# Kernel optimization log

Hardware: AMD Instinct MI355X
Metric: run time of the kernel (lower is better)

## Reference

```python
import jax, jax.numpy as jnp
import numpy as np

N_NODES = 50000
N_EDGES = 800000
NEG_SLOPE = 0.2


def _gat_layer(x, src, dst, W, a_src, a_dst, bias, heads, out_ch):
    """PyG-style GATConv with self-loops already appended to src/dst."""
    N = x.shape[0]
    h = (x @ W.T).reshape(N, heads, out_ch)            # [N,H,C]
    alpha_src = jnp.einsum('nhc,hc->nh', h, a_src)      # [N,H]
    alpha_dst = jnp.einsum('nhc,hc->nh', h, a_dst)      # [N,H]
    e = jax.nn.leaky_relu(alpha_src[src] + alpha_dst[dst], NEG_SLOPE)  # [E,H]
    # segment softmax over incoming edges of each destination node
    m = jax.ops.segment_max(e, dst, num_segments=N)     # [N,H]
    ex = jnp.exp(e - m[dst])
    denom = jax.ops.segment_sum(ex, dst, num_segments=N)  # [N,H] (>0: self-loops)
    alpha = ex / (denom[dst] + 1e-16)                    # [E,H]
    out = jax.ops.segment_sum(h[src] * alpha[:, :, None], dst, num_segments=N)  # [N,H,C]
    return out.reshape(N, heads * out_ch) + bias


def _with_self_loops(edge_index, n):
    loop = jnp.arange(n, dtype=edge_index.dtype)
    src = jnp.concatenate([edge_index[0], loop])
    dst = jnp.concatenate([edge_index[1], loop])
    return src, dst


def setup_inputs() -> dict:
    key = jax.random.key(0)
    ks = jax.random.split(key, 12)
    s = lambda fan: 1.0 / np.sqrt(fan)
    return {
        'x': jax.random.normal(ks[0], (N_NODES, 16), jnp.float32),
        'edge_index': jax.random.randint(ks[1], (2, N_EDGES), 0, N_NODES, jnp.int64),
        'W1': jax.random.normal(ks[2], (256, 16), jnp.float32) * s(16),
        'att_src1': jax.random.normal(ks[3], (4, 64), jnp.float32) * s(64),
        'att_dst1': jax.random.normal(ks[4], (4, 64), jnp.float32) * s(64),
        'b1': jnp.zeros((256,), jnp.float32),
        'W2': jax.random.normal(ks[5], (64, 256), jnp.float32) * s(256),
        'att_src2': jax.random.normal(ks[6], (1, 64), jnp.float32) * s(64),
        'att_dst2': jax.random.normal(ks[7], (1, 64), jnp.float32) * s(64),
        'b2': jnp.zeros((64,), jnp.float32),
        'fc_w': jax.random.normal(ks[8], (1, 64), jnp.float32) * s(64),
        'fc_b': jnp.zeros((1,), jnp.float32),
    }


def reference(x, edge_index, W1, att_src1, att_dst1, b1,
              W2, att_src2, att_dst2, b2, fc_w, fc_b):
    src, dst = _with_self_loops(edge_index, x.shape[0])
    h = jax.nn.elu(_gat_layer(x, src, dst, W1, att_src1, att_dst1, b1, heads=4, out_ch=64))
    h = jax.nn.elu(_gat_layer(h, src, dst, W2, att_src2, att_dst2, b2, heads=1, out_ch=64))
    return h @ fc_w.T + fc_b
```

## Files before the change

kernel.cpp:

```cpp
#include <hip/hip_runtime.h>
#include <hip/hip_bf16.h>
#include <stdint.h>

#define N_NODES 50000
#define N_EDGES 800000
#define MAXDEG  96
#define NSLICE  6250
#define NSB     196

#define OFF_X    0
#define OFF_W1   800000
#define OFF_AS1  804096
#define OFF_AD1  804352
#define OFF_B1   804608
#define OFF_W2   804864
#define OFF_AS2  821248
#define OFF_AD2  821312
#define OFF_B2   821376
#define OFF_FCW  821440
#define OFF_FCB  821504
#define N_CANON  821505
#define N_W2B    16384
#define N_W1B    16384
#define N_CONV   (N_CANON + N_W2B + N_W1B + N_NODES)

#define TSTRIDE 264

typedef __hip_bfloat16 bf16;
typedef __attribute__((ext_vector_type(8))) short short8;
typedef __attribute__((ext_vector_type(4))) float f32x4;

__device__ __forceinline__ float b2f(bf16 v){ return (float)v; }
__device__ __forceinline__ int clampi(int v, int lo, int hi){ return v < lo ? lo : (v > hi ? hi : v); }
__device__ __forceinline__ float clampf(float v){ return fminf(fmaxf(v, -40.f), 40.f); }
__device__ __forceinline__ uint16_t f2bfbits(float f){
  union { float f; uint32_t u; } c; c.f = f;
  uint32_t r = c.u + 0x7fff + ((c.u >> 16) & 1);
  return (uint16_t)(r >> 16);
}
__device__ __forceinline__ float bitsf(uint32_t u){
  union { uint32_t u; float f; } c; c.u = u; return c.f;
}
__device__ __forceinline__ uint32_t fbits(float f){
  union { float f; uint32_t u; } c; c.f = f; return c.u;
}

__device__ __forceinline__ int load_src(const int* ei, int i, int f){
  return f ? ei[2*(size_t)i] : ei[i];
}
__device__ __forceinline__ int load_dst(const int* ei, int i, int f){
  return f ? ei[2*((size_t)N_EDGES + i)] : ei[N_EDGES + i];
}

__global__ void k_detect(const int* __restrict__ ei, const uint16_t* __restrict__ xu,
                         int* __restrict__ flag){
  const int l = threadIdx.x;
  int or_odd = ei[2*l + 1] | ei[2*(400000 + l) + 1];
  int hits = 0;
  for(int k = 0; k < 64; k++){
    int e = (xu[l*64 + k] >> 7) & 0xFF;
    hits += (e >= 200);
  }
  #pragma unroll
  for(int off=32; off; off>>=1){
    or_odd |= __shfl_xor(or_odd, off, 64);
    hits   += __shfl_xor(hits,   off, 64);
  }
  if(l == 0){
    flag[0] = (or_odd == 0) ? 1 : 0;
    flag[1] = (hits > 16) ? 1 : 0;
  }
}

__global__ void k_convert(const void* x, const void* W1, const void* as1w, const void* ad1w,
                          const void* b1, const void* W2, const void* as2w, const void* ad2w,
                          const void* b2, const void* fcw, const void* fcb,
                          float* __restrict__ canon, uint16_t* __restrict__ W2b,
                          uint16_t* __restrict__ W1b, int* __restrict__ cnt,
                          int* __restrict__ csr_pad, const int* __restrict__ flag){
  int i = blockIdx.x*256 + threadIdx.x;
  int fp32 = flag[1];
  if(i >= N_CANON + N_W2B + N_W1B){
    int j = i - (N_CANON + N_W2B + N_W1B);
    if(j < N_NODES){ cnt[j] = 1; csr_pad[(size_t)j*MAXDEG] = j; }
    return;
  }
  if(i >= N_CANON + N_W2B){
    int j2 = i - (N_CANON + N_W2B);
    int j = j2 >> 6, kk = j2 & 63;
    uint16_t v = 0;
    if((kk >> 4) == (j >> 6)){
      int e = j*16 + (kk & 15);
      v = fp32 ? f2bfbits(((const float*)W1)[e]) : ((const uint16_t*)W1)[e];
    }
    W1b[j2] = v;
    return;
  }
  if(i >= N_CANON){
    int j = i - N_CANON;
    W2b[j] = fp32 ? f2bfbits(((const float*)W2)[j]) : ((const uint16_t*)W2)[j];
    return;
  }
  const void* src; int off;
  if     (i < OFF_W1 ){ src = x;    off = i; }
  else if(i < OFF_AS1){ src = W1;   off = i - OFF_W1; }
  else if(i < OFF_AD1){ src = as1w; off = i - OFF_AS1; }
  else if(i < OFF_B1 ){ src = ad1w; off = i - OFF_AD1; }
  else if(i < OFF_W2 ){ src = b1;   off = i - OFF_B1; }
  else if(i < OFF_AS2){ src = W2;   off = i - OFF_W2; }
  else if(i < OFF_AD2){ src = as2w; off = i - OFF_AS2; }
  else if(i < OFF_B2 ){ src = ad2w; off = i - OFF_AD2; }
  else if(i < OFF_FCW){ src = b2;   off = i - OFF_B2; }
  else if(i < OFF_FCB){ src = fcw;  off = i - OFF_FCW; }
  else               { src = fcb;  off = 0; }
  float v = fp32 ? ((const float*)src)[off] : b2f(((const bf16*)src)[off]);
  canon[i] = v;
}


__global__ __launch_bounds__(256) void k_prepscat(const float* __restrict__ canon,
                        uint32_t* __restrict__ pack, float* __restrict__ dpack,
                        const int* __restrict__ ei, int* __restrict__ cnt,
                        int* __restrict__ csr_pad, const int* __restrict__ flag){
  const int tid = threadIdx.x;
  if(blockIdx.x >= 196){
    const int bid = blockIdx.x - 196;
    const int grp = bid & 7, sb = bid >> 3;
    const int f = flag[0];
    const int lo = grp*NSLICE, hi = lo + NSLICE;
    const int base = sb*4096;
    #pragma unroll
    for(int j = 0; j < 8; j++){
      int i = base + j*512 + tid*2;
      if(i >= N_EDGES) break;
      int d0, d1;
      if(f){
        int4 dd = *(const int4*)(ei + 2*((size_t)N_EDGES + i));
        d0 = dd.x; d1 = dd.z;
      }else{
        int2 dd = *(const int2*)(ei + N_EDGES + i);
        d0 = dd.x; d1 = dd.y;
      }
      d0 = clampi(d0, 0, N_NODES-1);
      d1 = clampi(d1, 0, N_NODES-1);
      if(d0 >= lo && d0 < hi){
        int s = clampi(load_src(ei, i, f), 0, N_NODES-1);
        int pos = atomicAdd(&cnt[d0], 1);
        pos = clampi(pos, 0, MAXDEG-1);
        csr_pad[(size_t)d0*MAXDEG + pos] = s;
      }
      if(d1 >= lo && d1 < hi){
        int s = clampi(load_src(ei, i+1, f), 0, N_NODES-1);
        int pos = atomicAdd(&cnt[d1], 1);
        pos = clampi(pos, 0, MAXDEG-1);
        csr_pad[(size_t)d1*MAXDEG + pos] = s;
      }
    }
    return;
  }
  __shared__ float ps[64], pd[64];
  if(tid < 128){
    int e = tid & 63;
    int h = e >> 4, k = e & 15;
    const float* av = canon + (tid < 64 ? OFF_AS1 : OFF_AD1) + h*64;
    const float* Wp = canon + OFF_W1 + (h*64)*16 + k;
    float acc = 0.f;
    #pragma unroll 8
    for(int c = 0; c < 64; c++) acc += av[c] * Wp[c*16];
    (tid < 64 ? ps : pd)[e] = acc;
  }
  __syncthreads();
  int n = blockIdx.x*256 + tid;
  if(n >= N_NODES) return;
  float xr[16];
  const float4* xp = (const float4*)(canon + OFF_X + n*16);
  #pragma unroll
  for(int t=0;t<4;t++){ float4 v = xp[t]; xr[4*t]=v.x; xr[4*t+1]=v.y; xr[4*t+2]=v.z; xr[4*t+3]=v.w; }
  uint32_t w[16];
  #pragma unroll
  for(int t=0;t<8;t++)
    w[t] = (uint32_t)f2bfbits(xr[2*t]) | ((uint32_t)f2bfbits(xr[2*t+1]) << 16);
  float qs[8];
  #pragma unroll
  for(int h=0;h<4;h++){
    float a=0.f, b=0.f;
    #pragma unroll
    for(int k=0;k<16;k++){ a += ps[h*16+k]*xr[k]; b += pd[h*16+k]*xr[k]; }
    a = clampf(a); b = clampf(b);
    w[8+2*h]  = fbits(__expf(a));
    w[9+2*h]  = fbits(__expf(0.2f*a));
    qs[2*h]   = __expf(b);
    qs[2*h+1] = __expf(0.2f*b);
  }
  uint4* dst = (uint4*)(pack + (size_t)n*16);
  dst[0] = make_uint4(w[0],w[1],w[2],w[3]);
  dst[1] = make_uint4(w[4],w[5],w[6],w[7]);
  dst[2] = make_uint4(w[8],w[9],w[10],w[11]);
  dst[3] = make_uint4(w[12],w[13],w[14],w[15]);
  float4* dd = (float4*)(dpack + (size_t)n*8);
  dd[0] = make_float4(qs[0],qs[1],qs[2],qs[3]);
  dd[1] = make_float4(qs[4],qs[5],qs[6],qs[7]);
}


struct Ay { float y0,y1,y2,y3,d0,d1,d2,d3; };

__device__ __forceinline__ void edge_acc(const char* __restrict__ r, int k,
                                         float4 qa, float4 qb, bool valid, Ay& a){
  float xv = bitsf((uint32_t)(*(const uint16_t*)(r + k*2)) << 16);
  float4 pa = *(const float4*)(r + 32);
  float4 pb = *(const float4*)(r + 48);
  float w0 = fmaxf(pa.x*qa.x, pa.y*qa.y);
  float w1 = fmaxf(pa.z*qa.z, pa.w*qa.w);
  float w2 = fmaxf(pb.x*qb.x, pb.y*qb.y);
  float w3 = fmaxf(pb.z*qb.z, pb.w*qb.w);
  if(!valid){ w0 = 0.f; w1 = 0.f; w2 = 0.f; w3 = 0.f; }
  a.y0 += w0*xv; a.d0 += w0;
  a.y1 += w1*xv; a.d1 += w1;
  a.y2 += w2*xv; a.d2 += w2;
  a.y3 += w3*xv; a.d3 += w3;
}

__global__ __launch_bounds__(256) void k_aggy(const int* __restrict__ cnt, const int* __restrict__ csr_pad,
                       const uint32_t* __restrict__ pack, const float* __restrict__ dpack,
                       uint16_t* __restrict__ yb){
  const int wv = threadIdx.x >> 6, lane = threadIdx.x & 63;
  const int g = lane >> 4, k = lane & 15;
  const char* pk = (const char*)pack;

  for(int n = blockIdx.x*4 + wv; n < N_NODES; n += gridDim.x*4){
    const int beg = n*MAXDEG;
    const int deg = cnt[n];
    const int end = beg + (deg < MAXDEG ? deg : MAXDEG);
    const float4 qa = *(const float4*)(dpack + (size_t)n*8);
    const float4 qb = *(const float4*)(dpack + (size_t)n*8 + 4);
    Ay a = {0,0,0,0,0,0,0,0};
    int i0 = beg;
    const int nfull = (end - beg) >> 3;
    if(nfull > 0){
      int iA = csr_pad[i0 + g], iB = csr_pad[i0 + 4 + g];
      for(int b = 1; b < nfull; b++){
        int jA = csr_pad[i0 + 8 + g], jB = csr_pad[i0 + 12 + g];
        edge_acc(pk + (size_t)iA*64, k, qa, qb, true, a);
        edge_acc(pk + (size_t)iB*64, k, qa, qb, true, a);
        iA = jA; iB = jB;
        i0 += 8;
      }
      edge_acc(pk + (size_t)iA*64, k, qa, qb, true, a);
      edge_acc(pk + (size_t)iB*64, k, qa, qb, true, a);
      i0 += 8;
    }
    if(i0 < end){
      int iiA = i0 + g, iiB = i0 + 4 + g;
      bool vA = iiA < end, vB = iiB < end;
      int iA = csr_pad[vA ? iiA : end-1];
      int iB = csr_pad[vB ? iiB : end-1];
      edge_acc(pk + (size_t)iA*64, k, qa, qb, vA, a);
      edge_acc(pk + (size_t)iB*64, k, qa, qb, vB, a);
    }
    a.y0 += __shfl_xor(a.y0,16,64); a.y0 += __shfl_xor(a.y0,32,64);
    a.y1 += __shfl_xor(a.y1,16,64); a.y1 += __shfl_xor(a.y1,32,64);
    a.y2 += __shfl_xor(a.y2,16,64); a.y2 += __shfl_xor(a.y2,32,64);
    a.y3 += __shfl_xor(a.y3,16,64); a.y3 += __shfl_xor(a.y3,32,64);
    a.d0 += __shfl_xor(a.d0,16,64); a.d0 += __shfl_xor(a.d0,32,64);
    a.d1 += __shfl_xor(a.d1,16,64); a.d1 += __shfl_xor(a.d1,32,64);
    a.d2 += __shfl_xor(a.d2,16,64); a.d2 += __shfl_xor(a.d2,32,64);
    a.d3 += __shfl_xor(a.d3,16,64); a.d3 += __shfl_xor(a.d3,32,64);
    float yH = (g==0) ? a.y0 : (g==1) ? a.y1 : (g==2) ? a.y2 : a.y3;
    float dH = (g==0) ? a.d0 : (g==1) ? a.d1 : (g==2) ? a.d2 : a.d3;
    yb[(size_t)n*64 + g*16 + k] = f2bfbits(yH / (dH + 1e-16f));
  }
}


__global__ __launch_bounds__(64, 4) void k_mlp(const uint16_t* __restrict__ yb,
                        const uint16_t* __restrict__ W1b, const uint16_t* __restrict__ W2b,
                        const float* __restrict__ canon,
                        bf16* __restrict__ h2, float2* __restrict__ pq2, float2* __restrict__ dq2){
  __shared__ uint16_t tl[16*TSTRIDE];
  const int lane = threadIdx.x & 63;
  const int quad = lane >> 4, c = lane & 15;
  const int n0 = blockIdx.x * 16;

  float b1v[16];
  #pragma unroll
  for(int cb=0; cb<16; cb++) b1v[cb] = canon[OFF_B1 + cb*16 + c];
  float asj[4], adj[4];
  #pragma unroll
  for(int cb=0; cb<4; cb++){
    asj[cb] = canon[OFF_AS2 + cb*16 + c];
    adj[cb] = canon[OFF_AD2 + cb*16 + c];
  }

  short8 af0 = *(const short8*)(yb + (size_t)(n0 + c)*64 + quad*8);
  short8 af1 = *(const short8*)(yb + (size_t)(n0 + c)*64 + 32 + quad*8);
  #pragma unroll
  for(int cb=0; cb<16; cb++){
    short8 wf = *(const short8*)(W1b + (cb*16 + c)*64 + (cb>>3)*32 + quad*8);
    f32x4 acc = (f32x4){0.f,0.f,0.f,0.f};
    acc = __builtin_amdgcn_mfma_f32_16x16x32_bf16((cb>>3) ? af1 : af0, wf, acc, 0,0,0);
    #pragma unroll
    for(int r=0; r<4; r++){
      float o = acc[r] + b1v[cb];
      o = (o > 0.f) ? o : (__expf(o) - 1.f);
      tl[(quad*4 + r)*TSTRIDE + cb*16 + c] = f2bfbits(o);
    }
  }
  f32x4 acc2[4];
  #pragma unroll
  for(int cb=0; cb<4; cb++) acc2[cb] = (f32x4){0.f,0.f,0.f,0.f};
  #pragma unroll
  for(int ks=0; ks<8; ks++){
    short8 af = *(const short8*)(tl + c*TSTRIDE + ks*32 + quad*8);
    #pragma unroll
    for(int cb=0; cb<4; cb++){
      short8 bfrag = *(const short8*)(W2b + (cb*16 + c)*256 + ks*32 + quad*8);
      acc2[cb] = __builtin_amdgcn_mfma_f32_16x16x32_bf16(af, bfrag, acc2[cb], 0,0,0);
    }
  }
  float vs[4] = {0.f,0.f,0.f,0.f}, vd[4] = {0.f,0.f,0.f,0.f};
  #pragma unroll
  for(int cb=0; cb<4; cb++)
    #pragma unroll
    for(int r=0; r<4; r++){
      float v = acc2[cb][r];
      h2[(size_t)(n0 + quad*4 + r)*64 + cb*16 + c] = __float2bfloat16(v);
      vs[r] += v * asj[cb];
      vd[r] += v * adj[cb];
    }
  #pragma unroll
  for(int r=0; r<4; r++){
    #pragma unroll
    for(int off=1; off<16; off<<=1){
      vs[r] += __shfl_xor(vs[r], off, 64);
      vd[r] += __shfl_xor(vd[r], off, 64);
    }
  }
  if(c == 0){
    #pragma unroll
    for(int r=0; r<4; r++){
      float s = clampf(vs[r]), d = clampf(vd[r]);
      pq2[n0 + quad*4 + r] = make_float2(__expf(s), __expf(0.2f*s));
      dq2[n0 + quad*4 + r] = make_float2(__expf(d), __expf(0.2f*d));
    }
  }
}


__global__ __launch_bounds__(256) void k_agg2(const int* __restrict__ cnt, const int* __restrict__ csr_pad,
                       const bf16* __restrict__ h2, const float2* __restrict__ pq2,
                       const float2* __restrict__ dq2, const float* __restrict__ canon,
                       void* __restrict__ outv, const int* __restrict__ flag){
  const int wv = threadIdx.x >> 6, lane = threadIdx.x & 63;
  const int g = lane >> 4, k = lane & 15;
  const char* h2b = (const char*)h2;
  float4 b2v = ((const float4*)(canon + OFF_B2))[k];
  float4 fcv = ((const float4*)(canon + OFF_FCW))[k];
  const float fcb0 = canon[OFF_FCB];
  const int ofp32 = flag[1];
  for(int n = blockIdx.x*4 + wv; n < N_NODES; n += gridDim.x*4){
    const int beg = n*MAXDEG;
    int dg = cnt[n]; dg = dg < MAXDEG ? dg : MAXDEG;
    const int end = beg + dg;
    const float2 qn = dq2[n];
    float a0=0.f,a1=0.f,a2=0.f,a3=0.f, den=0.f;
    int i0 = beg;
    const int nfull = (end - beg) >> 3;
    if(nfull > 0){
      int iA = csr_pad[i0 + g], iB = csr_pad[i0 + 4 + g];
      for(int b = 1; b < nfull; b++){
        int nA = csr_pad[i0 + 8 + g], nB = csr_pad[i0 + 12 + g];
        uint2 hA = *(const uint2*)(h2b + (size_t)iA*128 + k*8);
        float2 pA = pq2[iA];
        uint2 hB = *(const uint2*)(h2b + (size_t)iB*128 + k*8);
        float2 pB = pq2[iB];
        float wA = fmaxf(pA.x*qn.x, pA.y*qn.y);
        float wB = fmaxf(pB.x*qn.x, pB.y*qn.y);
        den += wA + wB;
        a0 += wA*bitsf(hA.x << 16) + wB*bitsf(hB.x << 16);
        a1 += wA*bitsf(hA.x & 0xffff0000u) + wB*bitsf(hB.x & 0xffff0000u);
        a2 += wA*bitsf(hA.y << 16) + wB*bitsf(hB.y << 16);
        a3 += wA*bitsf(hA.y & 0xffff0000u) + wB*bitsf(hB.y & 0xffff0000u);
        iA = nA; iB = nB;
        i0 += 8;
      }
      {
        uint2 hA = *(const uint2*)(h2b + (size_t)iA*128 + k*8);
        float2 pA = pq2[iA];
        uint2 hB = *(const uint2*)(h2b + (size_t)iB*128 + k*8);
        float2 pB = pq2[iB];
        float wA = fmaxf(pA.x*qn.x, pA.y*qn.y);
        float wB = fmaxf(pB.x*qn.x, pB.y*qn.y);
        den += wA + wB;
        a0 += wA*bitsf(hA.x << 16) + wB*bitsf(hB.x << 16);
        a1 += wA*bitsf(hA.x & 0xffff0000u) + wB*bitsf(hB.x & 0xffff0000u);
        a2 += wA*bitsf(hA.y << 16) + wB*bitsf(hB.y << 16);
        a3 += wA*bitsf(hA.y & 0xffff0000u) + wB*bitsf(hB.y & 0xffff0000u);
        i0 += 8;
      }
    }
    if(i0 < end){
      int iiA = i0 + g, iiB = i0 + 4 + g;
      bool vA = iiA < end, vB = iiB < end;
      int iA = csr_pad[vA ? iiA : end-1];
      int iB = csr_pad[vB ? iiB : end-1];
      uint2 hA = *(const uint2*)(h2b + (size_t)iA*128 + k*8);
      float2 pA = pq2[iA];
      uint2 hB = *(const uint2*)(h2b + (size_t)iB*128 + k*8);
      float2 pB = pq2[iB];
      float wA = vA ? fmaxf(pA.x*qn.x, pA.y*qn.y) : 0.f;
      float wB = vB ? fmaxf(pB.x*qn.x, pB.y*qn.y) : 0.f;
      den += wA + wB;
      a0 += wA*bitsf(hA.x << 16) + wB*bitsf(hB.x << 16);
      a1 += wA*bitsf(hA.x & 0xffff0000u) + wB*bitsf(hB.x & 0xffff0000u);
      a2 += wA*bitsf(hA.y << 16) + wB*bitsf(hB.y << 16);
      a3 += wA*bitsf(hA.y & 0xffff0000u) + wB*bitsf(hB.y & 0xffff0000u);
    }
    a0 += __shfl_xor(a0,16,64); a0 += __shfl_xor(a0,32,64);
    a1 += __shfl_xor(a1,16,64); a1 += __shfl_xor(a1,32,64);
    a2 += __shfl_xor(a2,16,64); a2 += __shfl_xor(a2,32,64);
    a3 += __shfl_xor(a3,16,64); a3 += __shfl_xor(a3,32,64);
    den += __shfl_xor(den,16,64); den += __shfl_xor(den,32,64);
    float inv = 1.f/(den + 1e-16f);
    float o0 = a0*inv + b2v.x, o1 = a1*inv + b2v.y;
    float o2 = a2*inv + b2v.z, o3 = a3*inv + b2v.w;
    o0 = (o0>0.f)?o0:expm1f(o0); o1 = (o1>0.f)?o1:expm1f(o1);
    o2 = (o2>0.f)?o2:expm1f(o2); o3 = (o3>0.f)?o3:expm1f(o3);
    float v = o0*fcv.x + o1*fcv.y + o2*fcv.z + o3*fcv.w;
    v += __shfl_xor(v,1,64); v += __shfl_xor(v,2,64);
    v += __shfl_xor(v,4,64); v += __shfl_xor(v,8,64);
    if(lane == 0){
      float r = v + fcb0;
      if(ofp32) ((float*)outv)[n] = r;
      else      ((bf16*)outv)[n] = __float2bfloat16(r);
    }
  }
}


extern "C" void kernel_launch(void* const* d_in, const int* in_sizes, int n_in,
                              void* d_out, int out_size, void* d_ws, size_t ws_size,
                              hipStream_t stream){
  (void)in_sizes; (void)n_in; (void)out_size;
  const int* ei = (const int*)d_in[1];

  char* w = (char*)d_ws;
  auto carve = [&](size_t bytes)->char*{ char* p = w; w += (bytes + 255) & ~(size_t)255; return p; };
  int*      cnt     = (int*)     carve((size_t)N_NODES*4);
  int*      flag    = (int*)     carve(256);
  int*      csr_pad = (int*)     carve((size_t)N_NODES*MAXDEG*4);
  float*    canon   = (float*)   carve((size_t)N_CANON*4);
  uint16_t* W2b     = (uint16_t*)carve((size_t)N_W2B*2);
  uint16_t* W1b     = (uint16_t*)carve((size_t)N_W1B*2);
  uint32_t* pack    = (uint32_t*)carve((size_t)N_NODES*64);
  float*    dpack   = (float*)   carve((size_t)N_NODES*32);
  uint16_t* yb      = (uint16_t*)carve((size_t)N_NODES*64*2);
  float2*   pq2     = (float2*)  carve((size_t)N_NODES*8);
  float2*   dq2     = (float2*)  carve((size_t)N_NODES*8);
  bf16*     h2      = (bf16*)    carve((size_t)N_NODES*64*2);
  size_t required = (size_t)(w - (char*)d_ws);
  if(ws_size < required) return;

  hipLaunchKernelGGL(k_detect,   dim3(1), dim3(64), 0, stream, ei, (const uint16_t*)d_in[0], flag);
  hipLaunchKernelGGL(k_convert,  dim3((N_CONV+255)/256), dim3(256), 0, stream,
                     d_in[0], d_in[2], d_in[3], d_in[4], d_in[5], d_in[6], d_in[7], d_in[8],
                     d_in[9], d_in[10], d_in[11], canon, W2b, W1b, cnt, csr_pad, flag);
  hipLaunchKernelGGL(k_prepscat, dim3(196 + 8*NSB), dim3(256), 0, stream,
                     canon, pack, dpack, ei, cnt, csr_pad, flag);
  hipLaunchKernelGGL(k_aggy,     dim3(2048), dim3(256), 0, stream, cnt, csr_pad, pack, dpack, yb);
  hipLaunchKernelGGL(k_mlp,      dim3(N_NODES/16), dim3(64), 0, stream, yb, W1b, W2b, canon, h2, pq2, dq2);
  hipLaunchKernelGGL(k_agg2,     dim3(2048), dim3(256), 0, stream, cnt, csr_pad, h2, pq2, dq2, canon, d_out, flag);
}
```

Measured before the change: 199.6 us.

## Fuse conversion and prep/scatter kernels; handle self-loops inline in aggregation

Merges the input-conversion kernel and the prep/scatter kernel into one launch. The node-prep blocks now read raw x, W1 and the attention vectors directly in either fp32 or bf16, instead of waiting on the canonical fp32 copy. Counter zeroing moves into the detect kernel, and the self-loop is no longer written into the first CSR slot; both aggregation kernels add the self-loop contribution explicitly. This removes one kernel boundary and its serialization. In exchange, the prep blocks recompute conversions on the fly and the detect kernel grows to many blocks.

Result: no change. 199.2 us, median of 2 (-0.2%).

```diff
diff --git a/kernel.cpp b/kernel.cpp
--- a/kernel.cpp
+++ b/kernel.cpp
@@ -22,7 +22,12 @@
 #define N_CANON  821505
 #define N_W2B    16384
 #define N_W1B    16384
-#define N_CONV   (N_CANON + N_W2B + N_W1B + N_NODES)
+
+#define SCAT_BLKS (8*NSB)
+#define PACK_BLKS 196
+#define CONV_ELEMS (N_CANON + N_W2B + N_W1B)
+#define CONV_BLKS ((CONV_ELEMS + 255)/256)
+#define MEGA_BLKS (SCAT_BLKS + PACK_BLKS + CONV_BLKS)
 
 #define TSTRIDE 264
 
@@ -44,47 +49,142 @@
 __device__ __forceinline__ uint32_t fbits(float f){
   union { float f; uint32_t u; } c; c.f = f; return c.u;
 }
+__device__ __forceinline__ float ldf(const void* p, int i, int fp32){
+  return fp32 ? ((const float*)p)[i] : b2f(((const bf16*)p)[i]);
+}
 
 __device__ __forceinline__ int load_src(const int* ei, int i, int f){
   return f ? ei[2*(size_t)i] : ei[i];
 }
-__device__ __forceinline__ int load_dst(const int* ei, int i, int f){
-  return f ? ei[2*((size_t)N_EDGES + i)] : ei[N_EDGES + i];
-}
-
-__global__ void k_detect(const int* __restrict__ ei, const uint16_t* __restrict__ xu,
-                         int* __restrict__ flag){
-  const int l = threadIdx.x;
-  int or_odd = ei[2*l + 1] | ei[2*(400000 + l) + 1];
-  int hits = 0;
-  for(int k = 0; k < 64; k++){
-    int e = (xu[l*64 + k] >> 7) & 0xFF;
-    hits += (e >= 200);
-  }
-  #pragma unroll
-  for(int off=32; off; off>>=1){
-    or_odd |= __shfl_xor(or_odd, off, 64);
-    hits   += __shfl_xor(hits,   off, 64);
-  }
-  if(l == 0){
-    flag[0] = (or_odd == 0) ? 1 : 0;
-    flag[1] = (hits > 16) ? 1 : 0;
-  }
-}
-
-__global__ void k_convert(const void* x, const void* W1, const void* as1w, const void* ad1w,
-                          const void* b1, const void* W2, const void* as2w, const void* ad2w,
-                          const void* b2, const void* fcw, const void* fcb,
-                          float* __restrict__ canon, uint16_t* __restrict__ W2b,
-                          uint16_t* __restrict__ W1b, int* __restrict__ cnt,
-                          int* __restrict__ csr_pad, const int* __restrict__ flag){
-  int i = blockIdx.x*256 + threadIdx.x;
-  int fp32 = flag[1];
-  if(i >= N_CANON + N_W2B + N_W1B){
-    int j = i - (N_CANON + N_W2B + N_W1B);
-    if(j < N_NODES){ cnt[j] = 1; csr_pad[(size_t)j*MAXDEG] = j; }
+
+__global__ __launch_bounds__(256) void k_detect(const int* __restrict__ ei,
+                         const uint16_t* __restrict__ xu,
+                         int* __restrict__ flag, int* __restrict__ cnt){
+  const int gid = blockIdx.x*256 + threadIdx.x;
+  if(gid < N_NODES) cnt[gid] = 0;
+  if(blockIdx.x == 0 && threadIdx.x < 64){
+    const int l = threadIdx.x;
+    int or_odd = ei[2*l + 1] | ei[2*(400000 + l) + 1];
+    int hits = 0;
+    for(int k = 0; k < 64; k++){
+      int e = (xu[l*64 + k] >> 7) & 0xFF;
+      hits += (e >= 200);
+    }
+    #pragma unroll
+    for(int off=32; off; off>>=1){
+      or_odd |= __shfl_xor(or_odd, off, 64);
+      hits   += __shfl_xor(hits,   off, 64);
+    }
+    if(l == 0){
+      flag[0] = (or_odd == 0) ? 1 : 0;
+      flag[1] = (hits > 16) ? 1 : 0;
+    }
+  }
+}
+
+
+__global__ __launch_bounds__(256) void k_megaprep(
+    const void* x, const void* W1, const void* as1w, const void* ad1w,
+    const void* b1, const void* W2, const void* as2w, const void* ad2w,
+    const void* b2, const void* fcw, const void* fcb,
+    float* __restrict__ canon, uint16_t* __restrict__ W2b, uint16_t* __restrict__ W1b,
+    uint32_t* __restrict__ pack, float* __restrict__ dpack,
+    const int* __restrict__ ei, int* __restrict__ cnt, int* __restrict__ csr_pad,
+    const int* __restrict__ flag){
+  const int tid = threadIdx.x;
+
+  if(blockIdx.x < SCAT_BLKS){
+    const int bid = blockIdx.x;
+    const int grp = bid & 7, sb = bid >> 3;
+    const int f = flag[0];
+    const int lo = grp*NSLICE, hi = lo + NSLICE;
+    const int base = sb*4096;
+    #pragma unroll
+    for(int j = 0; j < 8; j++){
+      int i = base + j*512 + tid*2;
+      if(i >= N_EDGES) break;
+      int d0, d1;
+      if(f){
+        int4 dd = *(const int4*)(ei + 2*((size_t)N_EDGES + i));
+        d0 = dd.x; d1 = dd.z;
+      }else{
+        int2 dd = *(const int2*)(ei + N_EDGES + i);
+        d0 = dd.x; d1 = dd.y;
+      }
+      d0 = clampi(d0, 0, N_NODES-1);
+      d1 = clampi(d1, 0, N_NODES-1);
+      if(d0 >= lo && d0 < hi){
+        int s = clampi(load_src(ei, i, f), 0, N_NODES-1);
+        int pos = atomicAdd(&cnt[d0], 1);
+        pos = clampi(pos, 0, MAXDEG-1);
+        csr_pad[(size_t)d0*MAXDEG + pos] = s;
+      }
+      if(d1 >= lo && d1 < hi){
+        int s = clampi(load_src(ei, i+1, f), 0, N_NODES-1);
+        int pos = atomicAdd(&cnt[d1], 1);
+        pos = clampi(pos, 0, MAXDEG-1);
+        csr_pad[(size_t)d1*MAXDEG + pos] = s;
+      }
+    }
     return;
   }
+
+  if(blockIdx.x < SCAT_BLKS + PACK_BLKS){
+    const int fp32 = flag[1];
+    __shared__ float ps[64], pd[64];
+    if(tid < 128){
+      int e = tid & 63;
+      int h = e >> 4, kk = e & 15;
+      const void* av = (tid < 64) ? as1w : ad1w;
+      float acc = 0.f;
+      #pragma unroll 8
+      for(int c = 0; c < 64; c++)
+        acc += ldf(av, h*64 + c, fp32) * ldf(W1, (h*64 + c)*16 + kk, fp32);
+      (tid < 64 ? ps : pd)[e] = acc;
+    }
+    __syncthreads();
+    int n = (blockIdx.x - SCAT_BLKS)*256 + tid;
+    if(n >= N_NODES) return;
+    float xr[16];
+    if(fp32){
+      const float4* xp = (const float4*)((const float*)x + (size_t)n*16);
+      #pragma unroll
+      for(int t=0;t<4;t++){ float4 v = xp[t]; xr[4*t]=v.x; xr[4*t+1]=v.y; xr[4*t+2]=v.z; xr[4*t+3]=v.w; }
+    }else{
+      const uint16_t* xu16 = (const uint16_t*)x + (size_t)n*16;
+      #pragma unroll
+      for(int j=0;j<16;j++) xr[j] = bitsf((uint32_t)xu16[j] << 16);
+    }
+    uint32_t w[16];
+    #pragma unroll
+    for(int t=0;t<8;t++)
+      w[t] = (uint32_t)f2bfbits(xr[2*t]) | ((uint32_t)f2bfbits(xr[2*t+1]) << 16);
+    float qs[8];
+    #pragma unroll
+    for(int h=0;h<4;h++){
+      float a=0.f, b=0.f;
+      #pragma unroll
+      for(int kk=0;kk<16;kk++){ a += ps[h*16+kk]*xr[kk]; b += pd[h*16+kk]*xr[kk]; }
+      a = clampf(a); b = clampf(b);
+      w[8+2*h]  = fbits(__expf(a));
+      w[9+2*h]  = fbits(__expf(0.2f*a));
+      qs[2*h]   = __expf(b);
+      qs[2*h+1] = __expf(0.2f*b);
+    }
+    uint4* dst = (uint4*)(pack + (size_t)n*16);
+    dst[0] = make_uint4(w[0],w[1],w[2],w[3]);
+    dst[1] = make_uint4(w[4],w[5],w[6],w[7]);
+    dst[2] = make_uint4(w[8],w[9],w[10],w[11]);
+    dst[3] = make_uint4(w[12],w[13],w[14],w[15]);
+    float4* dd = (float4*)(dpack + (size_t)n*8);
+    dd[0] = make_float4(qs[0],qs[1],qs[2],qs[3]);
+    dd[1] = make_float4(qs[4],qs[5],qs[6],qs[7]);
+    return;
+  }
+
+  int i = (blockIdx.x - SCAT_BLKS - PACK_BLKS)*256 + tid;
+  if(i >= CONV_ELEMS) return;
+  const int fp32 = flag[1];
   if(i >= N_CANON + N_W2B){
     int j2 = i - (N_CANON + N_W2B);
     int j = j2 >> 6, kk = j2 & 63;
@@ -113,93 +213,7 @@
   else if(i < OFF_FCW){ src = b2;   off = i - OFF_B2; }
   else if(i < OFF_FCB){ src = fcw;  off = i - OFF_FCW; }
   else               { src = fcb;  off = 0; }
-  float v = fp32 ? ((const float*)src)[off] : b2f(((const bf16*)src)[off]);
-  canon[i] = v;
-}
-
-
-__global__ __launch_bounds__(256) void k_prepscat(const float* __restrict__ canon,
-                        uint32_t* __restrict__ pack, float* __restrict__ dpack,
-                        const int* __restrict__ ei, int* __restrict__ cnt,
-                        int* __restrict__ csr_pad, const int* __restrict__ flag){
-  const int tid = threadIdx.x;
-  if(blockIdx.x >= 196){
-    const int bid = blockIdx.x - 196;
-    const int grp = bid & 7, sb = bid >> 3;
-    const int f = flag[0];
-    const int lo = grp*NSLICE, hi = lo + NSLICE;
-    const int base = sb*4096;
-    #pragma unroll
-    for(int j = 0; j < 8; j++){
-      int i = base + j*512 + tid*2;
-      if(i >= N_EDGES) break;
-      int d0, d1;
-      if(f){
-        int4 dd = *(const int4*)(ei + 2*((size_t)N_EDGES + i));
-        d0 = dd.x; d1 = dd.z;
-      }else{
-        int2 dd = *(const int2*)(ei + N_EDGES + i);
-        d0 = dd.x; d1 = dd.y;
-      }
-      d0 = clampi(d0, 0, N_NODES-1);
-      d1 = clampi(d1, 0, N_NODES-1);
-      if(d0 >= lo && d0 < hi){
-        int s = clampi(load_src(ei, i, f), 0, N_NODES-1);
-        int pos = atomicAdd(&cnt[d0], 1);
-        pos = clampi(pos, 0, MAXDEG-1);
-        csr_pad[(size_t)d0*MAXDEG + pos] = s;
-      }
-      if(d1 >= lo && d1 < hi){
-        int s = clampi(load_src(ei, i+1, f), 0, N_NODES-1);
-        int pos = atomicAdd(&cnt[d1], 1);
-        pos = clampi(pos, 0, MAXDEG-1);
-        csr_pad[(size_t)d1*MAXDEG + pos] = s;
-      }
-    }
-    return;
-  }
-  __shared__ float ps[64], pd[64];
-  if(tid < 128){
-    int e = tid & 63;
-    int h = e >> 4, k = e & 15;
-    const float* av = canon + (tid < 64 ? OFF_AS1 : OFF_AD1) + h*64;
-    const float* Wp = canon + OFF_W1 + (h*64)*16 + k;
-    float acc = 0.f;
-    #pragma unroll 8
-    for(int c = 0; c < 64; c++) acc += av[c] * Wp[c*16];
-    (tid < 64 ? ps : pd)[e] = acc;
-  }
-  __syncthreads();
-  int n = blockIdx.x*256 + tid;
-  if(n >= N_NODES) return;
-  float xr[16];
-  const float4* xp = (const float4*)(canon + OFF_X + n*16);
-  #pragma unroll
-  for(int t=0;t<4;t++){ float4 v = xp[t]; xr[4*t]=v.x; xr[4*t+1]=v.y; xr[4*t+2]=v.z; xr[4*t+3]=v.w; }
-  uint32_t w[16];
-  #pragma unroll
-  for(int t=0;t<8;t++)
-    w[t] = (uint32_t)f2bfbits(xr[2*t]) | ((uint32_t)f2bfbits(xr[2*t+1]) << 16);
-  float qs[8];
-  #pragma unroll
-  for(int h=0;h<4;h++){
-    float a=0.f, b=0.f;
-    #pragma unroll
-    for(int k=0;k<16;k++){ a += ps[h*16+k]*xr[k]; b += pd[h*16+k]*xr[k]; }
-    a = clampf(a); b = clampf(b);
-    w[8+2*h]  = fbits(__expf(a));
-    w[9+2*h]  = fbits(__expf(0.2f*a));
-    qs[2*h]   = __expf(b);
-    qs[2*h+1] = __expf(0.2f*b);
-  }
-  uint4* dst = (uint4*)(pack + (size_t)n*16);
-  dst[0] = make_uint4(w[0],w[1],w[2],w[3]);
-  dst[1] = make_uint4(w[4],w[5],w[6],w[7]);
-  dst[2] = make_uint4(w[8],w[9],w[10],w[11]);
-  dst[3] = make_uint4(w[12],w[13],w[14],w[15]);
-  float4* dd = (float4*)(dpack + (size_t)n*8);
-  dd[0] = make_float4(qs[0],qs[1],qs[2],qs[3]);
-  dd[1] = make_float4(qs[4],qs[5],qs[6],qs[7]);
+  canon[i] = ldf(src, off, fp32);
 }
 
 
@@ -235,6 +249,7 @@
     const float4 qa = *(const float4*)(dpack + (size_t)n*8);
     const float4 qb = *(const float4*)(dpack + (size_t)n*8 + 4);
     Ay a = {0,0,0,0,0,0,0,0};
+    edge_acc(pk + (size_t)n*64, k, qa, qb, g == 0, a);
     int i0 = beg;
     const int nfull = (end - beg) >> 3;
     if(nfull > 0){
@@ -364,6 +379,16 @@
     const int end = beg + dg;
     const float2 qn = dq2[n];
     float a0=0.f,a1=0.f,a2=0.f,a3=0.f, den=0.f;
+    {
+      uint2 hS = *(const uint2*)(h2b + (size_t)n*128 + k*8);
+      float2 pS = pq2[n];
+      float wS = (g == 0) ? fmaxf(pS.x*qn.x, pS.y*qn.y) : 0.f;
+      den += wS;
+      a0 += wS*bitsf(hS.x << 16);
+      a1 += wS*bitsf(hS.x & 0xffff0000u);
+      a2 += wS*bitsf(hS.y << 16);
+      a3 += wS*bitsf(hS.y & 0xffff0000u);
+    }
     int i0 = beg;
     const int nfull = (end - beg) >> 3;
     if(nfull > 0){
@@ -461,12 +486,12 @@
   size_t required = (size_t)(w - (char*)d_ws);
   if(ws_size < required) return;
 
-  hipLaunchKernelGGL(k_detect,   dim3(1), dim3(64), 0, stream, ei, (const uint16_t*)d_in[0], flag);
-  hipLaunchKernelGGL(k_convert,  dim3((N_CONV+255)/256), dim3(256), 0, stream,
+  hipLaunchKernelGGL(k_detect,   dim3(196), dim3(256), 0, stream,
+                     ei, (const uint16_t*)d_in[0], flag, cnt);
+  hipLaunchKernelGGL(k_megaprep, dim3(MEGA_BLKS), dim3(256), 0, stream,
                      d_in[0], d_in[2], d_in[3], d_in[4], d_in[5], d_in[6], d_in[7], d_in[8],
-                     d_in[9], d_in[10], d_in[11], canon, W2b, W1b, cnt, csr_pad, flag);
-  hipLaunchKernelGGL(k_prepscat, dim3(196 + 8*NSB), dim3(256), 0, stream,
-                     canon, pack, dpack, ei, cnt, csr_pad, flag);
+                     d_in[9], d_in[10], d_in[11], canon, W2b, W1b, pack, dpack,
+                     ei, cnt, csr_pad, flag);
   hipLaunchKernelGGL(k_aggy,     dim3(2048), dim3(256), 0, stream, cnt, csr_pad, pack, dpack, yb);
   hipLaunchKernelGGL(k_mlp,      dim3(N_NODES/16), dim3(64), 0, stream, yb, W1b, W2b, canon, h2, pq2, dq2);
   hipLaunchKernelGGL(k_agg2,     dim3(2048), dim3(256), 0, stream, cnt, csr_pad, h2, pq2, dq2, canon, d_out, flag);
```
